# Optimization experiments

Measured on AMD Instinct MI355X. Metric: run time of the kernel, lower is better.

The kernel has to match this reference:

```python
import jax, jax.numpy as jnp
import numpy as np
import math

B, T, A, Z, E, H = 4, 16, 512, 512, 64, 8
HD = Z // H
NF = 6  # num Fourier freqs


def setup_inputs() -> dict:
    key = jax.random.key(0)
    ks = jax.random.split(key, 16)
    w = lambda k, shape: jax.random.normal(k, shape, jnp.float32) * 0.02
    return dict(
        z_current=jax.random.normal(ks[0], (B, A, Z), jnp.float32),
        z_pred=jax.random.normal(ks[1], (B, T, A, Z), jnp.float32),
        actions=jax.random.normal(ks[2], (B, T, 4), jnp.float32),
        Wq=w(ks[3], (Z, Z)), Wk=w(ks[4], (Z, Z)), Wv=w(ks[5], (Z, Z)),
        We=w(ks[6], (E, Z)), Wo=w(ks[7], (Z, Z)),
        g_lnq=jnp.ones((Z,), jnp.float32), b_lnq=jnp.zeros((Z,), jnp.float32),
        g_lno=jnp.ones((Z,), jnp.float32), b_lno=jnp.zeros((Z,), jnp.float32),
        W_ff1=w(ks[8], (Z, 4 * Z)), b_ff1=jnp.zeros((4 * Z,), jnp.float32),
        W_ff2=w(ks[9], (4 * Z, Z)), b_ff2=jnp.zeros((Z,), jnp.float32),
        W_edge=w(ks[10], (3 * 2 * NF + 2, E)), b_edge=jnp.zeros((E,), jnp.float32),
        Wg1=w(ks[11], (2 * Z, Z)), bg1=jnp.zeros((Z,), jnp.float32),
        Wg2=w(ks[12], (Z, 1)), bg2=jnp.zeros((1,), jnp.float32),
    )


def _ln(x, g, b, eps=1e-5):
    m = jnp.mean(x, -1, keepdims=True)
    v = jnp.var(x, -1, keepdims=True)
    return (x - m) * jax.lax.rsqrt(v + eps) * g + b


def _fourier(a3):
    # a3: [B,T,3] -> [B,T, 2 + 6*NF]
    dx, dy, th = a3[..., 0:1], a3[..., 1:2], a3[..., 2:3]
    feats = [jnp.sin(th), jnp.cos(th)]
    for k in range(NF):
        f = (2.0 ** k) * math.pi
        feats += [jnp.sin(f * dx), jnp.cos(f * dx),
                  jnp.sin(f * dy), jnp.cos(f * dy),
                  jnp.sin(f * th), jnp.cos(f * th)]
    return jnp.concatenate(feats, -1)


def reference(z_current, z_pred, actions, Wq, Wk, Wv, We, Wo,
              g_lnq, b_lnq, g_lno, b_lno, W_ff1, b_ff1, W_ff2, b_ff2,
              W_edge, b_edge, Wg1, bg1, Wg2, bg2):
    q = _ln(z_pred, g_lnq, b_lnq) @ Wq                      # [B,T,A,Z]
    kc = z_current @ Wk                                      # [B,A,Z]
    vc = z_current @ Wv                                      # [B,A,Z]
    e = (_fourier(actions[..., :3]) @ W_edge + b_edge) @ We  # [B,T,Z]
    k = kc[:, None, :, :] + e[:, :, None, :]                 # [B,T,A,Z] (edge-biased keys)

    qh = q.reshape(B, T, A, H, HD)
    kh = k.reshape(B, T, A, H, HD)
    vh = vc.reshape(B, A, H, HD)

    # Non-standard attention: outer product over head INDEX (i,j in [0,H)),
    # elementwise along head_dim d -> logits [B,T,A,HD,H,H]
    logits = jnp.einsum('btaid,btajd->btadij', qh, kh) / math.sqrt(HD)
    attn = jax.lax.stop_gradient(jax.nn.softmax(logits, axis=-1))  # torch @no_grad softmax
    out_h = jnp.einsum('btadij,bajd->btaid', attn, vh)       # [B,T,A,H,HD]
    out = out_h.reshape(B, T, A, Z) @ Wo

    gate_inp = jnp.concatenate([out, z_pred], -1)            # [B,T,A,2Z]
    g = jax.nn.sigmoid(
        jax.nn.gelu(gate_inp @ Wg1 + bg1, approximate=False) @ Wg2 + bg2)  # [B,T,A,1]

    z_mid = _ln(z_pred + g * out, g_lno, b_lno)
    return z_mid + (jax.nn.gelu(z_mid @ W_ff1 + b_ff1, approximate=False) @ W_ff2 + b_ff2)
```

## Files before the change

kernel.cpp:

```cpp
#include <hip/hip_runtime.h>
#include <hip/hip_bf16.h>
#include <math.h>


typedef __bf16 bf16x8 __attribute__((ext_vector_type(8)));
typedef float f32x4 __attribute__((ext_vector_type(4)));

#define ROWS 32768
#define ZDIM 512

__device__ __forceinline__ void gload16(const void* gptr, void* ldsptr) {
  __builtin_amdgcn_global_load_lds(
      (const __attribute__((address_space(1))) unsigned int*)gptr,
      (__attribute__((address_space(3))) unsigned int*)ldsptr, 16, 0, 0);
}

__device__ __forceinline__ float gelu_f(float x) {
  return 0.5f * x * (1.0f + erff(x * 0.70710678118654752f));
}

__global__ void transpose_f32_bf16(const float* __restrict__ in,
                                   __bf16* __restrict__ out, int R, int C) {
  __shared__ float tile[32][33];
  int c0 = blockIdx.x * 32, r0 = blockIdx.y * 32;
#pragma unroll
  for (int i = 0; i < 32; i += 8)
    tile[i + threadIdx.y][threadIdx.x] =
        in[(size_t)(r0 + i + threadIdx.y) * C + c0 + threadIdx.x];
  __syncthreads();
#pragma unroll
  for (int i = 0; i < 32; i += 8)
    out[(size_t)(c0 + i + threadIdx.y) * R + r0 + threadIdx.x] =
        (__bf16)tile[threadIdx.x][i + threadIdx.y];
}

__global__ void cvt_f32_bf16(const float* __restrict__ in,
                             __bf16* __restrict__ out) {
  int i = (blockIdx.x * 256 + threadIdx.x) * 4;
  float4 v = *(const float4*)(in + i);
  out[i + 0] = (__bf16)v.x;
  out[i + 1] = (__bf16)v.y;
  out[i + 2] = (__bf16)v.z;
  out[i + 3] = (__bf16)v.w;
}

template <bool GATED, bool EMIT_RAW>
__global__ __launch_bounds__(256) void ln_kernel(
    const float* __restrict__ xa, const __bf16* __restrict__ xb,
    const float* __restrict__ gate, const float* __restrict__ gamma,
    const float* __restrict__ beta, __bf16* __restrict__ out,
    __bf16* __restrict__ raw) {
  int row = blockIdx.x;
  int tid = threadIdx.x;
  int i0 = tid * 2;
  const float* ra = xa + (size_t)row * ZDIM;
  float x0 = ra[i0], x1 = ra[i0 + 1];
  if (EMIT_RAW) {
    raw[(size_t)row * ZDIM + i0] = (__bf16)x0;
    raw[(size_t)row * ZDIM + i0 + 1] = (__bf16)x1;
  }
  if (GATED) {
    float gv = gate[row];
    const __bf16* rb = xb + (size_t)row * ZDIM;
    x0 += gv * (float)rb[i0];
    x1 += gv * (float)rb[i0 + 1];
  }
  float s = x0 + x1, s2 = x0 * x0 + x1 * x1;
#pragma unroll
  for (int off = 32; off > 0; off >>= 1) {
    s += __shfl_down(s, off);
    s2 += __shfl_down(s2, off);
  }
  __shared__ float red[8];
  int wave = tid >> 6, lane = tid & 63;
  if (lane == 0) { red[wave] = s; red[4 + wave] = s2; }
  __syncthreads();
  float ts = red[0] + red[1] + red[2] + red[3];
  float ts2 = red[4] + red[5] + red[6] + red[7];
  float mean = ts * (1.0f / ZDIM);
  float var = ts2 * (1.0f / ZDIM) - mean * mean;
  float rstd = rsqrtf(var + 1e-5f);
  float y0 = (x0 - mean) * rstd * gamma[i0] + beta[i0];
  float y1 = (x1 - mean) * rstd * gamma[i0 + 1] + beta[i0 + 1];
  out[(size_t)row * ZDIM + i0] = (__bf16)y0;
  out[(size_t)row * ZDIM + i0 + 1] = (__bf16)y1;
}

__global__ void edge_kernel(const float* __restrict__ actions,
                            const float* __restrict__ W_edge,
                            const float* __restrict__ b_edge,
                            const float* __restrict__ We,
                            float* __restrict__ e) {
  int bt = blockIdx.x;
  int tid = threadIdx.x;
  float dx = actions[bt * 4 + 0];
  float dy = actions[bt * 4 + 1];
  float th = actions[bt * 4 + 2];
  float feats[38];
  feats[0] = sinf(th);
  feats[1] = cosf(th);
  int idx = 2;
  float f = 3.14159265358979323846f;
#pragma unroll
  for (int k = 0; k < 6; k++) {
    feats[idx++] = sinf(f * dx);
    feats[idx++] = cosf(f * dx);
    feats[idx++] = sinf(f * dy);
    feats[idx++] = cosf(f * dy);
    feats[idx++] = sinf(f * th);
    feats[idx++] = cosf(f * th);
    f *= 2.0f;
  }
  __shared__ float hid[64];
  float h = b_edge[tid];
  for (int ff = 0; ff < 38; ff++) h += feats[ff] * W_edge[ff * 64 + tid];
  hid[tid] = h;
  __syncthreads();
#pragma unroll
  for (int i = 0; i < 8; i++) {
    int z = i * 64 + tid;
    float sacc = 0.0f;
    for (int j = 0; j < 64; j++) sacc += hid[j] * We[j * ZDIM + z];
    e[(size_t)bt * ZDIM + z] = sacc;
  }
}

__global__ __launch_bounds__(256) void attn_kernel(
    const __bf16* __restrict__ q, const __bf16* __restrict__ kvc,
    const float* __restrict__ e, __bf16* __restrict__ attn_out) {
  int row = blockIdx.x * 4 + (threadIdx.x >> 6);
  int lane = threadIdx.x & 63;
  int a = row & 511;
  int bt = row >> 9;
  int b = bt >> 4;
  const __bf16* qr = q + (size_t)row * ZDIM;
  const __bf16* kr = kvc + ((size_t)b * 512 + a) * 1024;
  const __bf16* vr = kr + 512;
  const float* er = e + (size_t)bt * ZDIM;
  float kv[8], vv[8], qv[8];
#pragma unroll
  for (int j = 0; j < 8; j++) {
    kv[j] = (float)kr[j * 64 + lane] + er[j * 64 + lane];
    vv[j] = (float)vr[j * 64 + lane];
  }
#pragma unroll
  for (int i = 0; i < 8; i++) qv[i] = (float)qr[i * 64 + lane];
  const float scale = 0.125f;
#pragma unroll
  for (int i = 0; i < 8; i++) {
    float lg[8], m = -1e30f;
#pragma unroll
    for (int j = 0; j < 8; j++) {
      lg[j] = qv[i] * kv[j] * scale;
      m = fmaxf(m, lg[j]);
    }
    float ssum = 0.0f, o = 0.0f;
#pragma unroll
    for (int j = 0; j < 8; j++) {
      float p = __expf(lg[j] - m);
      ssum += p;
      o += p * vv[j];
    }
    attn_out[(size_t)row * ZDIM + i * 64 + lane] = (__bf16)(o / ssum);
  }
}

__global__ __launch_bounds__(256) void gate_kernel(
    const __bf16* __restrict__ hg, const float* __restrict__ Wg2,
    const float* __restrict__ bg2, float* __restrict__ g) {
  int row = blockIdx.x * 4 + (threadIdx.x >> 6);
  int lane = threadIdx.x & 63;
  float s = 0.0f;
#pragma unroll
  for (int i = 0; i < 8; i++) {
    int z = i * 64 + lane;
    s += (float)hg[(size_t)row * ZDIM + z] * Wg2[z];
  }
#pragma unroll
  for (int off = 32; off > 0; off >>= 1) s += __shfl_down(s, off);
  if (lane == 0) g[row] = 1.0f / (1.0f + expf(-(s + bg2[0])));
}

template <bool CONCAT, int EPI, typename OT>
__global__ __launch_bounds__(256) void gemm_kernel(
    const __bf16* __restrict__ A1, const __bf16* __restrict__ A2, int ksplit,
    int lda, const __bf16* __restrict__ Bt, const float* __restrict__ bias,
    const __bf16* __restrict__ resid, OT* __restrict__ C, int N, int K) {
  __shared__ __align__(16) __bf16 As[3][128 * 32];
  __shared__ __align__(16) __bf16 Bs[3][128 * 32];
  const int tid = threadIdx.x;
  const int wave = tid >> 6, lane = tid & 63;
  const int nwg = gridDim.x * gridDim.y;
  const int bid = blockIdx.x + gridDim.x * blockIdx.y;
  const int sw = (bid & 7) * (nwg >> 3) + (bid >> 3);
  const int nN = gridDim.y;
  const int m0 = (sw / nN) * 128, n0 = (sw % nN) * 128;
  const int srow = lane >> 2;
  const int scol = (lane & 3) * 8;
  const int wm = (wave & 1) * 64, wn = (wave >> 1) * 64;
  const int fr = lane & 15, fq = lane >> 4;

  f32x4 acc[4][4] = {};

  auto stage = [&](int buf, int kt) {
    const __bf16* Ap;
    int ka;
    if (CONCAT) {
      if (kt < ksplit) { Ap = A1; ka = kt; }
      else             { Ap = A2; ka = kt - ksplit; }
    } else { Ap = A1; ka = kt; }
#pragma unroll
    for (int c = 0; c < 2; c++) {
      int r = 32 * wave + 16 * c + srow;
      gload16(Ap + (size_t)(m0 + r) * lda + ka + scol,
              &As[buf][(32 * wave + 16 * c) * 32]);
      gload16(Bt + (size_t)(n0 + r) * K + kt + scol,
              &Bs[buf][(32 * wave + 16 * c) * 32]);
    }
  };

  const int nk = K >> 5;
  stage(0, 0);
  stage(1, 32);
  int buf = 0;
  for (int t = 0; t < nk; ++t) {
    if (t + 1 < nk) asm volatile("s_waitcnt vmcnt(4)" ::: "memory");
    else            asm volatile("s_waitcnt vmcnt(0)" ::: "memory");
    __builtin_amdgcn_s_barrier();
    __builtin_amdgcn_sched_barrier(0);

    if (t + 2 < nk) {
      int nb = buf + 2; if (nb >= 3) nb -= 3;
      stage(nb, (t + 2) << 5);
    }

    bf16x8 af[4], bfr[4];
#pragma unroll
    for (int x = 0; x < 4; x++) {
      af[x] = *(const bf16x8*)&As[buf][(wm + x * 16 + fr) * 32 + fq * 8];
      bfr[x] = *(const bf16x8*)&Bs[buf][(wn + x * 16 + fr) * 32 + fq * 8];
    }
#pragma unroll
    for (int mt = 0; mt < 4; mt++)
#pragma unroll
      for (int nt = 0; nt < 4; nt++)
        acc[mt][nt] = __builtin_amdgcn_mfma_f32_16x16x32_bf16(
            af[mt], bfr[nt], acc[mt][nt], 0, 0, 0);

    __builtin_amdgcn_sched_barrier(0);
    buf = (buf == 2) ? 0 : buf + 1;
  }

#pragma unroll
  for (int mt = 0; mt < 4; mt++) {
#pragma unroll
    for (int nt = 0; nt < 4; nt++) {
      int col = n0 + wn + nt * 16 + fr;
#pragma unroll
      for (int r = 0; r < 4; r++) {
        int row = m0 + wm + mt * 16 + fq * 4 + r;
        float v = acc[mt][nt][r];
        if (EPI == 1) { v = gelu_f(v + bias[col]); }
        else if (EPI == 2) {
          v += bias[col] + (float)resid[(size_t)row * N + col];
        }
        C[(size_t)row * N + col] = (OT)v;
      }
    }
  }
}

extern "C" void kernel_launch(void* const* d_in, const int* in_sizes, int n_in,
                              void* d_out, int out_size, void* d_ws,
                              size_t ws_size, hipStream_t stream) {
  const float* z_current = (const float*)d_in[0];
  const float* z_pred = (const float*)d_in[1];
  const float* actions = (const float*)d_in[2];
  const float* Wq = (const float*)d_in[3];
  const float* Wk = (const float*)d_in[4];
  const float* Wv = (const float*)d_in[5];
  const float* We = (const float*)d_in[6];
  const float* Wo = (const float*)d_in[7];
  const float* g_lnq = (const float*)d_in[8];
  const float* b_lnq = (const float*)d_in[9];
  const float* g_lno = (const float*)d_in[10];
  const float* b_lno = (const float*)d_in[11];
  const float* W_ff1 = (const float*)d_in[12];
  const float* b_ff1 = (const float*)d_in[13];
  const float* W_ff2 = (const float*)d_in[14];
  const float* b_ff2 = (const float*)d_in[15];
  const float* W_edge = (const float*)d_in[16];
  const float* b_edge = (const float*)d_in[17];
  const float* Wg1 = (const float*)d_in[18];
  const float* bg1 = (const float*)d_in[19];
  const float* Wg2 = (const float*)d_in[20];
  const float* bg2 = (const float*)d_in[21];

  char* ws = (char*)d_ws;
  size_t off = 0;
  auto alloc = [&](size_t bytes) {
    void* p = ws + off;
    off += (bytes + 255) & ~(size_t)255;
    return p;
  };
  __bf16* WTkv = (__bf16*)alloc(1024 * 512 * 2);
  __bf16* WTq = (__bf16*)alloc(512 * 512 * 2);
  __bf16* WTo = (__bf16*)alloc(512 * 512 * 2);
  __bf16* WTg1 = (__bf16*)alloc(512 * 1024 * 2);
  __bf16* WTf1 = (__bf16*)alloc(2048 * 512 * 2);
  __bf16* WTf2 = (__bf16*)alloc(512 * 2048 * 2);
  __bf16* zc_bf = (__bf16*)alloc(2048 * 512 * 2);
  __bf16* zp_bf = (__bf16*)alloc((size_t)ROWS * ZDIM * 2);
  __bf16* kvc = (__bf16*)alloc(2048 * 1024 * 2);
  float* ebuf = (float*)alloc(64 * 512 * 4);
  float* gbuf = (float*)alloc(32768 * 4);
  __bf16* BUF_A = (__bf16*)alloc((size_t)2 * ROWS * ZDIM * 2);
  __bf16* BUF_B = BUF_A + (size_t)ROWS * ZDIM;
  __bf16* BUF_C = (__bf16*)alloc((size_t)ROWS * ZDIM * 2);
  (void)ws_size; (void)in_sizes; (void)n_in; (void)out_size;

  dim3 tb(32, 8);
  transpose_f32_bf16<<<dim3(16, 16), tb, 0, stream>>>(Wk, WTkv, 512, 512);
  transpose_f32_bf16<<<dim3(16, 16), tb, 0, stream>>>(Wv, WTkv + 512 * 512,
                                                      512, 512);
  transpose_f32_bf16<<<dim3(16, 16), tb, 0, stream>>>(Wq, WTq, 512, 512);
  transpose_f32_bf16<<<dim3(16, 16), tb, 0, stream>>>(Wo, WTo, 512, 512);
  transpose_f32_bf16<<<dim3(16, 32), tb, 0, stream>>>(Wg1, WTg1, 1024, 512);
  transpose_f32_bf16<<<dim3(64, 16), tb, 0, stream>>>(W_ff1, WTf1, 512, 2048);
  transpose_f32_bf16<<<dim3(16, 64), tb, 0, stream>>>(W_ff2, WTf2, 2048, 512);

  cvt_f32_bf16<<<1024, 256, 0, stream>>>(z_current, zc_bf);
  ln_kernel<false, true><<<ROWS, 256, 0, stream>>>(z_pred, nullptr, nullptr,
                                                   g_lnq, b_lnq, BUF_A, zp_bf);
  edge_kernel<<<64, 64, 0, stream>>>(actions, W_edge, b_edge, We, ebuf);
  gemm_kernel<false, 0, __bf16><<<dim3(16, 8), 256, 0, stream>>>(
      zc_bf, nullptr, 0, 512, WTkv, nullptr, nullptr, kvc, 1024, 512);
  gemm_kernel<false, 0, __bf16><<<dim3(256, 4), 256, 0, stream>>>(
      BUF_A, nullptr, 0, 512, WTq, nullptr, nullptr, BUF_B, 512, 512);
  attn_kernel<<<ROWS / 4, 256, 0, stream>>>(BUF_B, kvc, ebuf, BUF_A);
  gemm_kernel<false, 0, __bf16><<<dim3(256, 4), 256, 0, stream>>>(
      BUF_A, nullptr, 0, 512, WTo, nullptr, nullptr, BUF_B, 512, 512);
  gemm_kernel<true, 1, __bf16><<<dim3(256, 4), 256, 0, stream>>>(
      BUF_B, zp_bf, 512, 512, WTg1, bg1, nullptr, BUF_C, 512, 1024);
  gate_kernel<<<ROWS / 4, 256, 0, stream>>>(BUF_C, Wg2, bg2, gbuf);
  ln_kernel<true, false><<<ROWS, 256, 0, stream>>>(z_pred, BUF_B, gbuf, g_lno,
                                                   b_lno, BUF_C, nullptr);
  float* outp = (float*)d_out;
  __bf16* h1 = BUF_A;
  for (int c = 0; c < 2; c++) {
    const __bf16* zmid_c = BUF_C + (size_t)c * 16384 * 512;
    gemm_kernel<false, 1, __bf16><<<dim3(128, 16), 256, 0, stream>>>(
        zmid_c, nullptr, 0, 512, WTf1, b_ff1, nullptr, h1, 2048, 512);
    gemm_kernel<false, 2, float><<<dim3(128, 4), 256, 0, stream>>>(
        h1, nullptr, 0, 2048, WTf2, b_ff2, zmid_c,
        outp + (size_t)c * 16384 * 512, 512, 2048);
  }
}
```

Baseline: 653.6 us.

## Load GEMM B fragments directly from global into registers instead of LDS

The B operand is no longer staged through a triple-buffered LDS tile. Each wave now loads its own B fragments straight from global memory into double-buffered registers, two k-steps ahead. The wait count is raised so the extra in-flight loads stay pending. This halves LDS usage and removes the LDS reads for B, but waves that share a B tile now load it twice. Each global access covers only 64 contiguous bytes per row, and the extra registers may reduce occupancy.

```diff
diff --git a/kernel.cpp b/kernel.cpp
--- a/kernel.cpp
+++ b/kernel.cpp
@@ -187,7 +187,6 @@
     int lda, const __bf16* __restrict__ Bt, const float* __restrict__ bias,
     const __bf16* __restrict__ resid, OT* __restrict__ C, int N, int K) {
   __shared__ __align__(16) __bf16 As[3][128 * 32];
-  __shared__ __align__(16) __bf16 Bs[3][128 * 32];
   const int tid = threadIdx.x;
   const int wave = tid >> 6, lane = tid & 63;
   const int nwg = gridDim.x * gridDim.y;
@@ -202,7 +201,7 @@
 
   f32x4 acc[4][4] = {};
 
-  auto stage = [&](int buf, int kt) {
+  auto stageA = [&](int buf, int kt) {
     const __bf16* Ap;
     int ka;
     if (CONCAT) {
@@ -214,38 +213,57 @@
       int r = 32 * wave + 16 * c + srow;
       gload16(Ap + (size_t)(m0 + r) * lda + ka + scol,
               &As[buf][(32 * wave + 16 * c) * 32]);
-      gload16(Bt + (size_t)(n0 + r) * K + kt + scol,
-              &Bs[buf][(32 * wave + 16 * c) * 32]);
     }
   };
 
+  const __bf16* Bbase = Bt + (size_t)(n0 + wn + fr) * K + fq * 8;
+  auto loadB = [&](bf16x8 b[4], int kt) {
+#pragma unroll
+    for (int x = 0; x < 4; x++)
+      b[x] = *(const bf16x8*)(Bbase + (size_t)(x * 16) * K + kt);
+  };
+
   const int nk = K >> 5;
-  stage(0, 0);
-  stage(1, 32);
+  bf16x8 b0[4], b1[4];
+  stageA(0, 0);
+  loadB(b0, 0);
+  stageA(1, 32);
+  loadB(b1, 32);
+
   int buf = 0;
   for (int t = 0; t < nk; ++t) {
-    if (t + 1 < nk) asm volatile("s_waitcnt vmcnt(4)" ::: "memory");
+    if (t + 1 < nk) asm volatile("s_waitcnt vmcnt(6)" ::: "memory");
     else            asm volatile("s_waitcnt vmcnt(0)" ::: "memory");
     __builtin_amdgcn_s_barrier();
     __builtin_amdgcn_sched_barrier(0);
 
     if (t + 2 < nk) {
       int nb = buf + 2; if (nb >= 3) nb -= 3;
-      stage(nb, (t + 2) << 5);
-    }
-
-    bf16x8 af[4], bfr[4];
-#pragma unroll
-    for (int x = 0; x < 4; x++) {
+      stageA(nb, (t + 2) << 5);
+    }
+
+    bf16x8 af[4];
+#pragma unroll
+    for (int x = 0; x < 4; x++)
       af[x] = *(const bf16x8*)&As[buf][(wm + x * 16 + fr) * 32 + fq * 8];
-      bfr[x] = *(const bf16x8*)&Bs[buf][(wn + x * 16 + fr) * 32 + fq * 8];
-    }
-#pragma unroll
-    for (int mt = 0; mt < 4; mt++)
-#pragma unroll
-      for (int nt = 0; nt < 4; nt++)
-        acc[mt][nt] = __builtin_amdgcn_mfma_f32_16x16x32_bf16(
-            af[mt], bfr[nt], acc[mt][nt], 0, 0, 0);
+
+    if (t & 1) {
+#pragma unroll
+      for (int mt = 0; mt < 4; mt++)
+#pragma unroll
+        for (int nt = 0; nt < 4; nt++)
+          acc[mt][nt] = __builtin_amdgcn_mfma_f32_16x16x32_bf16(
+              af[mt], b1[nt], acc[mt][nt], 0, 0, 0);
+      if (t + 2 < nk) loadB(b1, (t + 2) << 5);
+    } else {
+#pragma unroll
+      for (int mt = 0; mt < 4; mt++)
+#pragma unroll
+        for (int nt = 0; nt < 4; nt++)
+          acc[mt][nt] = __builtin_amdgcn_mfma_f32_16x16x32_bf16(
+              af[mt], b0[nt], acc[mt][nt], 0, 0, 0);
+      if (t + 2 < nk) loadB(b0, (t + 2) << 5);
+    }
 
     __builtin_amdgcn_sched_barrier(0);
     buf = (buf == 2) ? 0 : buf + 1;
```

After: 964.8 us. 1.48x slower.
